# Kernel tuning notes

Hardware: AMD Instinct MI355X
Metric: run time of the kernel (lower is better)

The kernel has to match this reference:

```python
import jax, jax.numpy as jnp
import numpy as np

B = 8          # events
P = 16384      # points per event (P > MAX_TOKENS -> selection path)
FEAT = 6
TOK = 768
MT = 128       # max_tokens
K = 16         # k_neighbors
IH = 256       # importance_hidden_dim
LN_EPS = 1e-5


def _linear_init(key, fan_in, fan_out):
    kw, kb = jax.random.split(key)
    lim = 1.0 / np.sqrt(fan_in)
    w = jax.random.uniform(kw, (fan_in, fan_out), jnp.float32, -lim, lim)
    b = jax.random.uniform(kb, (fan_out,), jnp.float32, -lim, lim)
    return w, b


def setup_inputs() -> dict:
    key = jax.random.key(0)
    ks = jax.random.split(key, 16)
    # point data: col0 = batch index (sorted, equal counts), cols1:5 = x,y,z,t
    xyzt = jax.random.normal(ks[0], (B * P, 4), jnp.float32)
    bidx = jnp.repeat(jnp.arange(B, dtype=jnp.float32), P)[:, None]
    coordinates = jnp.concatenate([bidx, xyzt], axis=-1)
    features = jax.random.normal(ks[1], (B * P, FEAT), jnp.float32)
    # gumbel noise = -log(-log(U+1e-10)+1e-10)
    u = jax.random.uniform(ks[2], (B, P), jnp.float32)
    gumbel_noise = -jnp.log(-jnp.log(u + 1e-10) + 1e-10)
    # feature MLP: 6->256->512->768 (ReLU) -> 768
    w1, b1 = _linear_init(ks[3], FEAT, 256)
    w2, b2 = _linear_init(ks[4], 256, 512)
    w3, b3 = _linear_init(ks[5], 512, 768)
    w4, b4 = _linear_init(ks[6], 768, TOK)
    # importance encoder: (768+4)->256, ReLU, LN, 256->256, ReLU, 256->1
    iw1, ib1 = _linear_init(ks[7], TOK + 4, IH)
    ln_g = jnp.ones((IH,), jnp.float32)
    ln_b = jnp.zeros((IH,), jnp.float32)
    iw2, ib2 = _linear_init(ks[8], IH, IH)
    iw3, ib3 = _linear_init(ks[9], IH, 1)
    # neighborhood MLP: 768->768, ReLU, 768->768
    nw1, nb1 = _linear_init(ks[10], TOK, TOK)
    nw2, nb2 = _linear_init(ks[11], TOK, TOK)
    log_temperature = jnp.zeros((), jnp.float32)  # log(1.0)
    return dict(coordinates=coordinates, features=features,
                log_temperature=log_temperature,
                w1=w1, b1=b1, w2=w2, b2=b2, w3=w3, b3=b3, w4=w4, b4=b4,
                iw1=iw1, ib1=ib1, ln_g=ln_g, ln_b=ln_b, iw2=iw2, ib2=ib2,
                iw3=iw3, ib3=ib3, nw1=nw1, nb1=nb1, nw2=nw2, nb2=nb2,
                gumbel_noise=gumbel_noise, batch_size=B)


def _forward(coordinates, features, log_temperature,
             w1, b1, w2, b2, w3, b3, w4, b4,
             iw1, ib1, ln_g, ln_b, iw2, ib2, iw3, ib3,
             nw1, nb1, nw2, nb2, gumbel_noise, batch_size):
    N = coordinates.shape[0]
    Pn = N // batch_size
    coords4 = coordinates[:, 1:5]  # [N,4] (x,y,z,t)
    # point feature MLP
    h = jax.nn.relu(features @ w1 + b1)
    h = jax.nn.relu(h @ w2 + b2)
    h = jax.nn.relu(h @ w3 + b3)
    pf = h @ w4 + b4  # [N, TOK]
    # importance scores (context-aware)
    z = jax.nn.relu(jnp.concatenate([pf, coords4], axis=-1) @ iw1 + ib1)
    mu = jnp.mean(z, axis=-1, keepdims=True)
    var = jnp.var(z, axis=-1, keepdims=True)
    z = (z - mu) / jnp.sqrt(var + LN_EPS) * ln_g + ln_b
    z = jax.nn.relu(z @ iw2 + ib2)
    imp = (z @ iw3 + ib3)[:, 0]  # [N]
    temp = jnp.maximum(jnp.exp(log_temperature), 0.1)
    # equal-count sorted batches -> reshape and vmap over events
    pf_b = pf.reshape(batch_size, Pn, TOK)
    c_b = coords4.reshape(batch_size, Pn, 4)
    imp_b = imp.reshape(batch_size, Pn)

    def per_event(feats, coords, scores, noise):
        # gumbel-softmax top-k selection (soft mode: weights unused downstream)
        pert = (scores + noise) / temp
        _, sel = jax.lax.top_k(pert, MT)            # [MT]
        cent = coords[sel]                           # [MT,4]
        # squared euclidean distances centroids -> all points (same KNN order as cdist)
        d2 = jnp.sum((cent[:, None, :] - coords[None, :, :]) ** 2, axis=-1)  # [MT,P]
        _, knn = jax.lax.top_k(-d2, K)               # [MT,K]
        nbr = feats[knn]                             # [MT,K,TOK]
        pooled = jnp.max(nbr, axis=1)                # [MT,TOK]
        tok = jax.nn.relu(pooled @ nw1 + nb1) @ nw2 + nb2
        order = jnp.argsort(cent[:, 3])              # sort tokens by time
        return tok[order], cent[order]

    tokens, cents = jax.vmap(per_event)(pf_b, c_b, imp_b, gumbel_noise)
    return tokens, cents


def reference(coordinates, features, log_temperature,
              w1, b1, w2, b2, w3, b3, w4, b4,
              iw1, ib1, ln_g, ln_b, iw2, ib2, iw3, ib3,
              nw1, nb1, nw2, nb2, gumbel_noise, batch_size):
    tokens, cents = _forward(coordinates, features, log_temperature,
                             w1, b1, w2, b2, w3, b3, w4, b4,
                             iw1, ib1, ln_g, ln_b, iw2, ib2, iw3, ib3,
                             nw1, nb1, nw2, nb2, gumbel_noise, batch_size)
    masks = jnp.ones((batch_size, MT), dtype=bool)  # all events have > MT points
    return tokens, cents, masks
```

## Files before the change

kernel.cpp:

```cpp
#include <hip/hip_runtime.h>
#include <hip/hip_bf16.h>

#define NPT   131072
#define BATCH 8
#define PPE   16384
#define MT    128
#define KNN   16
#define TOKD  768
#define ZSPLIT 2

typedef short bf16x8 __attribute__((ext_vector_type(8)));
typedef float f32x4  __attribute__((ext_vector_type(4)));

#define GL16(g, l) __builtin_amdgcn_global_load_lds(                         \
    (const __attribute__((address_space(1))) void*)(g),                      \
    (__attribute__((address_space(3))) void*)(l), 16, 0, 0)

__device__ __forceinline__ unsigned pack_hi(unsigned u0, unsigned u1) {
    return (u0 >> 16) | (u1 & 0xFFFF0000u);
}
__device__ __forceinline__ void split1(float x, short& h, short& l) {
    const unsigned u = __float_as_uint(x);
    h = (short)(u >> 16);
    const float r = x - __uint_as_float(u & 0xFFFF0000u);
    l = (short)(__float_as_uint(r) >> 16);
}

__global__ __launch_bounds__(256) void prep_kernel(const float* __restrict__ coords,
                                                   float4* __restrict__ c4f)
{
    const int i = blockIdx.x * 256 + threadIdx.x;
    if (i < NPT) {
        const long b = (long)i * 5;
        c4f[i] = make_float4(coords[b + 1], coords[b + 2], coords[b + 3], coords[b + 4]);
    }
}

__global__ __launch_bounds__(256) void wsplit_all(
    const float* __restrict__ w2, const float* __restrict__ w3,
    const float* __restrict__ w4, const float* __restrict__ iw2,
    const float* __restrict__ nw1, const float* __restrict__ nw2,
    short* w2h, short* w2l, short* w3h, short* w3l,
    short* w4h, short* w4l, short* i2h, short* i2l,
    short* n1h, short* n1l, short* n2h, short* n2l)
{
    const int b = blockIdx.x;
    const float* W; int K, N, Kpad, n; short *hi, *lo;
    if (b < 512)       { W = w2;  K = 256; N = 512; Kpad = 256; hi = w2h; lo = w2l; n = b; }
    else if (b < 1280) { W = w3;  K = 512; N = 768; Kpad = 512; hi = w3h; lo = w3l; n = b - 512; }
    else if (b < 2048) { W = w4;  K = 768; N = 768; Kpad = 768; hi = w4h; lo = w4l; n = b - 1280; }
    else if (b < 2304) { W = iw2; K = 256; N = 256; Kpad = 256; hi = i2h; lo = i2l; n = b - 2048; }
    else if (b < 3072) { W = nw1; K = 768; N = 768; Kpad = 768; hi = n1h; lo = n1l; n = b - 2304; }
    else               { W = nw2; K = 768; N = 768; Kpad = 768; hi = n2h; lo = n2l; n = b - 3072; }
    for (int k = threadIdx.x; k < Kpad; k += 256) {
        short h = 0, l = 0;
        if (k < K) split1(W[(long)k * N + n], h, l);
        hi[(long)n * Kpad + k] = h;
        lo[(long)n * Kpad + k] = l;
    }
}

__global__ __launch_bounds__(256) void w45_kernel(const float* __restrict__ w4,
                                                  const float* __restrict__ iw1,
                                                  const float* __restrict__ b4,
                                                  const float* __restrict__ ib1,
                                                  short* __restrict__ hi,
                                                  short* __restrict__ lo,
                                                  float* __restrict__ bias45)
{
    const int k = blockIdx.x, n = threadIdx.x;
    if (k < 768) {
        const float* wr = w4 + (long)k * 768;
        float v0 = 0.f, v1 = 0.f, v2 = 0.f, v3 = 0.f;
        for (int j = 0; j < 768; j += 4) {
            v0 += wr[j]     * iw1[(long)j * 256 + n];
            v1 += wr[j + 1] * iw1[(long)(j + 1) * 256 + n];
            v2 += wr[j + 2] * iw1[(long)(j + 2) * 256 + n];
            v3 += wr[j + 3] * iw1[(long)(j + 3) * 256 + n];
        }
        const float v = (v0 + v1) + (v2 + v3);
        short h, l; split1(v, h, l);
        hi[(long)n * 800 + k] = h;
        lo[(long)n * 800 + k] = l;
    } else if (k < 800) {
        const float v = (k < 772) ? iw1[(long)k * 256 + n] : 0.f;
        short h, l; split1(v, h, l);
        hi[(long)n * 800 + k] = h;
        lo[(long)n * 800 + k] = l;
    } else {
        float v0 = 0.f, v1 = 0.f, v2 = 0.f, v3 = 0.f;
        for (int j = 0; j < 768; j += 4) {
            v0 += b4[j]     * iw1[(long)j * 256 + n];
            v1 += b4[j + 1] * iw1[(long)(j + 1) * 256 + n];
            v2 += b4[j + 2] * iw1[(long)(j + 2) * 256 + n];
            v3 += b4[j + 3] * iw1[(long)(j + 3) * 256 + n];
        }
        bias45[n] = (v0 + v1) + (v2 + v3) + ib1[n];
    }
}

__global__ __launch_bounds__(256) void l1_kernel(const float* __restrict__ f,
                                                 const float* __restrict__ w1,
                                                 const float* __restrict__ b1,
                                                 short* __restrict__ hp,
                                                 short* __restrict__ lp,
                                                 int base,
                                                 const int* __restrict__ gather)
{
    const int r0 = blockIdx.x << 6, tid = threadIdx.x;
    float wc[6];
#pragma unroll
    for (int k = 0; k < 6; ++k) wc[k] = w1[k * 256 + tid];
    const float bb = b1[tid];
    for (int i = 0; i < 64; ++i) {
        const int r = r0 + i;
        int row = gather ? gather[r] : (base + r);
        row = (row < 0) ? 0 : ((row >= NPT) ? (NPT - 1) : row);
        float acc = bb;
#pragma unroll
        for (int k = 0; k < 6; ++k) acc += f[(long)row * 6 + k] * wc[k];
        acc = fmaxf(acc, 0.f);
        short h, l; split1(acc, h, l);
        hp[(long)r * 256 + tid] = h;
        lp[(long)r * 256 + tid] = l;
    }
}

__global__ __launch_bounds__(256) void gather_h3_kernel(const short* __restrict__ H3,
                                                        const int* __restrict__ knn_idx,
                                                        int off,
                                                        short* __restrict__ G)
{
    const int i = blockIdx.x;
    const int row = knn_idx[off + i];
    const int4* src = (const int4*)(H3 + (long)row * 768);
    int4* dst = (int4*)(G + (long)i * 768);
    if (threadIdx.x < 96) dst[threadIdx.x] = src[threadIdx.x];
}

__global__ __launch_bounds__(256, 3) void gemm_mf(
    const short* __restrict__ Aph, const short* __restrict__ Apl,
    const float* __restrict__ Afp, int Kpad,
    const short* __restrict__ Wth, const short* __restrict__ Wtl,
    const float* __restrict__ bias,
    short* __restrict__ Cph, short* __restrict__ Cpl, int KpadOut,
    float* __restrict__ Cf, short* __restrict__ Cp768,
    float* __restrict__ Cpool,
    const float* __restrict__ CoordC, int cfBase,
    int N, int relu, long partStride)
{
    __shared__ short Ah[128 * 32];
    __shared__ short Al[128 * 32];
    __shared__ short Bh[128 * 32];
    __shared__ short Bl[128 * 32];
    const int tid = threadIdx.x;
    int rowb, colb;
    {
        const int ncol = gridDim.x, nrow = gridDim.y;
        if ((nrow & 7) == 0) {
            const int id  = blockIdx.y * ncol + blockIdx.x;
            const int sgs = ncol << 3;
            const int sg = id / sgs, wi = id % sgs;
            rowb = (sg << 3) + (wi & 7);
            colb = wi >> 3;
        } else { rowb = blockIdx.y; colb = blockIdx.x; }
    }
    const int row0 = rowb << 7, col0 = colb << 7;
    const int wave = tid >> 6, lane = tid & 63;
    const int wr = wave >> 1, wc = wave & 1;
    const int q = lane >> 4, l16 = lane & 15;
    const int l2 = lane >> 2;
    const int ksw = (((lane & 3) ^ ((lane >> 3) & 3)) << 3);
    const int rchunk = ((q ^ ((l16 >> 1) & 3)) << 3);

    f32x4 acc[4][4];
#pragma unroll
    for (int mt = 0; mt < 4; ++mt)
#pragma unroll
        for (int nt = 0; nt < 4; ++nt)
            acc[mt][nt] = (f32x4){0.f, 0.f, 0.f, 0.f};

    const bool useAl = (Apl != nullptr) || (Aph == nullptr);
    const int nkT = Kpad >> 5;
    const int Z = gridDim.z, zb = blockIdx.z;
    const int t0 = (nkT * zb) / Z, t1 = (nkT * (zb + 1)) / Z;

    auto stage = [&](int t) {
        const int k0 = t << 5;
#pragma unroll
        for (int i = 0; i < 2; ++i) {
            const int mb = (wave << 5) + (i << 4);
            const long gb = (long)(col0 + mb + l2) * Kpad + k0 + ksw;
            GL16(&Wth[gb], &Bh[mb * 32]);
            GL16(&Wtl[gb], &Bl[mb * 32]);
        }
        if (Aph) {
#pragma unroll
            for (int i = 0; i < 2; ++i) {
                const int mb = (wave << 5) + (i << 4);
                const long ga = (long)(row0 + mb + l2) * Kpad + k0 + ksw;
                GL16(&Aph[ga], &Ah[mb * 32]);
                if (Apl) GL16(&Apl[ga], &Al[mb * 32]);
            }
        } else {
#pragma unroll
            for (int s = 0; s < 4; ++s) {
                const int l  = (s << 8) + tid;
                const int m  = l >> 3;
                const int k4 = (l & 7) << 2;
                const float4 v = *(const float4*)&Afp[(long)(row0 + m) * Kpad + k0 + k4];
                const unsigned u0 = __float_as_uint(v.x), u1 = __float_as_uint(v.y);
                const unsigned u2 = __float_as_uint(v.z), u3 = __float_as_uint(v.w);
                const unsigned r0 = __float_as_uint(v.x - __uint_as_float(u0 & 0xFFFF0000u));
                const unsigned r1 = __float_as_uint(v.y - __uint_as_float(u1 & 0xFFFF0000u));
                const unsigned r2 = __float_as_uint(v.z - __uint_as_float(u2 & 0xFFFF0000u));
                const unsigned r3 = __float_as_uint(v.w - __uint_as_float(u3 & 0xFFFF0000u));
                const int off = m * 32 + ((((k4 >> 3) ^ ((m >> 1) & 3)) << 3) | (k4 & 4));
                *(int2*)&Ah[off] = make_int2((int)pack_hi(u0, u1), (int)pack_hi(u2, u3));
                *(int2*)&Al[off] = make_int2((int)pack_hi(r0, r1), (int)pack_hi(r2, r3));
            }
        }
    };

    stage(t0);
    __syncthreads();

    for (int t = t0; t < t1; ++t) {
        bf16x8 ah[4], al[4], bh[4], bl[4];
#pragma unroll
        for (int i = 0; i < 4; ++i) {
            const int mrow = (wr << 6) + (i << 4) + l16;
            const int ncol = (wc << 6) + (i << 4) + l16;
            ah[i] = *(const bf16x8*)&Ah[mrow * 32 + rchunk];
            if (useAl) al[i] = *(const bf16x8*)&Al[mrow * 32 + rchunk];
            bh[i] = *(const bf16x8*)&Bh[ncol * 32 + rchunk];
            bl[i] = *(const bf16x8*)&Bl[ncol * 32 + rchunk];
        }
        __syncthreads();
        if (t + 1 < t1) stage(t + 1);
#pragma unroll
        for (int nt = 0; nt < 4; ++nt)
#pragma unroll
            for (int mt = 0; mt < 4; ++mt) {
                acc[mt][nt] = __builtin_amdgcn_mfma_f32_16x16x32_bf16(ah[mt], bh[nt], acc[mt][nt], 0, 0, 0);
                acc[mt][nt] = __builtin_amdgcn_mfma_f32_16x16x32_bf16(ah[mt], bl[nt], acc[mt][nt], 0, 0, 0);
                if (useAl)
                    acc[mt][nt] = __builtin_amdgcn_mfma_f32_16x16x32_bf16(al[mt], bh[nt], acc[mt][nt], 0, 0, 0);
            }
        __syncthreads();
    }

    if (Cf && Z > 1) {
        float* dst = Cf + (long)zb * partStride;
#pragma unroll
        for (int mt = 0; mt < 4; ++mt)
#pragma unroll
            for (int nt = 0; nt < 4; ++nt) {
                const int col = col0 + (wc << 6) + (nt << 4) + l16;
#pragma unroll
                for (int rg = 0; rg < 4; ++rg) {
                    const int row = row0 + (wr << 6) + (mt << 4) + (q << 2) + rg;
                    dst[(long)row * N + col] = acc[mt][nt][rg];
                }
            }
        return;
    }

    if (Cpool) {
#pragma unroll
        for (int mt = 0; mt < 4; ++mt)
#pragma unroll
            for (int nt = 0; nt < 4; ++nt) {
                const int col = col0 + (wc << 6) + (nt << 4) + l16;
                float m = fmaxf(fmaxf(acc[mt][nt][0], acc[mt][nt][1]),
                                fmaxf(acc[mt][nt][2], acc[mt][nt][3]));
                m = fmaxf(m, __shfl_xor(m, 16));
                m = fmaxf(m, __shfl_xor(m, 32));
                m += bias[col];
                if (relu) m = fmaxf(m, 0.f);
                if (q == 0)
                    Cpool[(long)((row0 >> 4) + (wr << 2) + mt) * 768 + col] = m;
            }
        return;
    }
#pragma unroll
    for (int mt = 0; mt < 4; ++mt)
#pragma unroll
        for (int nt = 0; nt < 4; ++nt) {
            const int col = col0 + (wc << 6) + (nt << 4) + l16;
            const float bs = bias[col];
#pragma unroll
            for (int rg = 0; rg < 4; ++rg) {
                const int row = row0 + (wr << 6) + (mt << 4) + (q << 2) + rg;
                float v = acc[mt][nt][rg] + bs;
                if (relu) v = fmaxf(v, 0.f);
                if (Cf) Cf[(long)row * N + col] = v;
                if (Cph || Cp768) {
                    short h, l; split1(v, h, l);
                    if (Cph) {
                        Cph[(long)row * KpadOut + col] = h;
                        Cpl[(long)row * KpadOut + col] = l;
                    }
                    if (Cp768) Cp768[(long)row * 768 + col] = h;
                }
            }
        }
    if (CoordC && Cph && colb == 0 && tid < 128) {
        const int r = row0 + tid;
        const long rb = (long)r * KpadOut;
        const long cb = (long)(cfBase + r) * 5;
#pragma unroll
        for (int d = 0; d < 4; ++d) {
            short h, l; split1(CoordC[cb + 1 + d], h, l);
            Cph[rb + 768 + d] = h;
            Cpl[rb + 768 + d] = l;
        }
        for (int c = 772; c < 800; ++c) { Cph[rb + c] = 0; Cpl[rb + c] = 0; }
    }
}

__global__ __launch_bounds__(256) void ln_kernel(const float* __restrict__ Fp,
                                                 long pstride,
                                                 const float* __restrict__ g,
                                                 const float* __restrict__ b,
                                                 const float* __restrict__ badd,
                                                 short* __restrict__ hp,
                                                 short* __restrict__ lp)
{
    const int tid = threadIdx.x, wave = tid >> 6, lane = tid & 63;
    float gv[4], bv[4], av[4];
#pragma unroll
    for (int j = 0; j < 4; ++j) {
        gv[j] = g[lane * 4 + j]; bv[j] = b[lane * 4 + j]; av[j] = badd[lane * 4 + j];
    }
    for (int i = 0; i < 2; ++i) {
        const int r = (blockIdx.x << 3) + (wave << 1) + i;
        const long off = (long)r * 256 + lane * 4;
        float4 x = *(const float4*)&Fp[off];
#pragma unroll
        for (int z = 1; z < ZSPLIT; ++z) {
            const float4 p = *(const float4*)&Fp[(long)z * pstride + off];
            x.x += p.x; x.y += p.y; x.z += p.z; x.w += p.w;
        }
        x.x = fmaxf(x.x + av[0], 0.f);
        x.y = fmaxf(x.y + av[1], 0.f);
        x.z = fmaxf(x.z + av[2], 0.f);
        x.w = fmaxf(x.w + av[3], 0.f);
        float s = x.x + x.y + x.z + x.w;
#pragma unroll
        for (int off2 = 32; off2; off2 >>= 1) s += __shfl_down(s, off2);
        const float mu = __shfl(s, 0) * (1.f / 256.f);
        const float d0 = x.x - mu, d1 = x.y - mu, d2 = x.z - mu, d3 = x.w - mu;
        float s2 = d0 * d0 + d1 * d1 + d2 * d2 + d3 * d3;
#pragma unroll
        for (int off2 = 32; off2; off2 >>= 1) s2 += __shfl_down(s2, off2);
        const float den = sqrtf(__shfl(s2, 0) * (1.f / 256.f) + 1e-5f);
        const float v[4] = { d0 / den * gv[0] + bv[0], d1 / den * gv[1] + bv[1],
                             d2 / den * gv[2] + bv[2], d3 / den * gv[3] + bv[3] };
#pragma unroll
        for (int j = 0; j < 4; ++j) {
            short h, l; split1(v[j], h, l);
            hp[(long)r * 256 + lane * 4 + j] = h;
            lp[(long)r * 256 + lane * 4 + j] = l;
        }
    }
}

__global__ __launch_bounds__(256) void imp_kernel(const float* __restrict__ Fp,
                                                  long pstride,
                                                  const float* __restrict__ iw3,
                                                  const float* __restrict__ ib3,
                                                  const float* __restrict__ ib2,
                                                  const float* __restrict__ noise,
                                                  const float* __restrict__ lt,
                                                  float* __restrict__ pert,
                                                  int base)
{
    const int tid = threadIdx.x, wave = tid >> 6, lane = tid & 63;
    float wv[4], bv[4];
#pragma unroll
    for (int j = 0; j < 4; ++j) { wv[j] = iw3[lane * 4 + j]; bv[j] = ib2[lane * 4 + j]; }
    const float temp = fmaxf(expf(lt[0]), 0.1f);
    const float b3v = ib3[0];
    for (int i = 0; i < 2; ++i) {
        const int r = (blockIdx.x << 3) + (wave << 1) + i;
        const long off = (long)r * 256 + lane * 4;
        float4 x = *(const float4*)&Fp[off];
#pragma unroll
        for (int z = 1; z < ZSPLIT; ++z) {
            const float4 p = *(const float4*)&Fp[(long)z * pstride + off];
            x.x += p.x; x.y += p.y; x.z += p.z; x.w += p.w;
        }
        float s = fmaxf(x.x + bv[0], 0.f) * wv[0] + fmaxf(x.y + bv[1], 0.f) * wv[1]
                + fmaxf(x.z + bv[2], 0.f) * wv[2] + fmaxf(x.w + bv[3], 0.f) * wv[3];
#pragma unroll
        for (int off2 = 32; off2; off2 >>= 1) s += __shfl_down(s, off2);
        if (lane == 0)
            pert[base + r] = (s + b3v + noise[base + r]) / temp;
    }
}

__device__ __forceinline__ unsigned fmap(float f) {
    unsigned x = __float_as_uint(f);
    return (x & 0x80000000u) ? ~x : (x | 0x80000000u);
}

__global__ __launch_bounds__(256) void topk_part(const float* __restrict__ pert,
                                                 unsigned long long* __restrict__ cand)
{
    const int e = blockIdx.x >> 3, s = blockIdx.x & 7, tid = threadIdx.x;
    const int base = e * PPE + s * 2048;
    __shared__ unsigned long long key[2048];
    for (int i = tid; i < 2048; i += 256)
        key[i] = ((unsigned long long)fmap(pert[base + i]) << 32) | (unsigned)(~(base + i));
    __syncthreads();
    for (int k = 2; k <= 2048; k <<= 1)
        for (int j = k >> 1; j > 0; j >>= 1) {
            for (int i = tid; i < 2048; i += 256) {
                const int l = i ^ j;
                if (l > i) {
                    const unsigned long long a = key[i], b = key[l];
                    const bool up = ((i & k) == 0);
                    if (up ? (a < b) : (a > b)) { key[i] = b; key[l] = a; }
                }
            }
            __syncthreads();
        }
    if (tid < MT) cand[(long)blockIdx.x * MT + tid] = key[tid];
}

__global__ __launch_bounds__(256) void topk_merge(const unsigned long long* __restrict__ cand,
                                                  const float4* __restrict__ c4f,
                                                  float* __restrict__ centf)
{
    const int e = blockIdx.x, tid = threadIdx.x;
    __shared__ unsigned long long key[1024];
    for (int i = tid; i < 1024; i += 256)
        key[i] = cand[(long)e * 1024 + i];
    __syncthreads();
    for (int k = 2; k <= 1024; k <<= 1)
        for (int j = k >> 1; j > 0; j >>= 1) {
            for (int i = tid; i < 1024; i += 256) {
                const int l = i ^ j;
                if (l > i) {
                    const unsigned long long a = key[i], b = key[l];
                    const bool up = ((i & k) == 0);
                    if (up ? (a < b) : (a > b)) { key[i] = b; key[l] = a; }
                }
            }
            __syncthreads();
        }
    if (tid < MT) {
        const int idx = (int)(~(unsigned)(key[tid] & 0xFFFFFFFFu));
        *(float4*)&centf[(long)(e * MT + tid) * 4] = c4f[idx];
    }
}

__device__ __forceinline__ unsigned d2bits(const float4 x, float c0, float c1,
                                           float c2, float c3) {
    const float q0 = __fmul_rn(c0 - x.x, c0 - x.x);
    const float q1 = __fmul_rn(c1 - x.y, c1 - x.y);
    const float q2 = __fmul_rn(c2 - x.z, c2 - x.z);
    const float q3 = __fmul_rn(c3 - x.w, c3 - x.w);
    return __float_as_uint(__fadd_rn(__fadd_rn(__fadd_rn(q0, q1), q2), q3));
}

__global__ __launch_bounds__(256) void knn_kernel(const float4* __restrict__ c4f,
                                                  const float* __restrict__ centf,
                                                  int* __restrict__ knn_idx)
{
    const int blk = blockIdx.x, tid = threadIdx.x;
    const int e = blk >> 7, base = e * PPE;
    const int c4 = tid & 3;
    const float c0 = centf[(long)blk * 4 + 0];
    const float c1 = centf[(long)blk * 4 + 1];
    const float c2 = centf[(long)blk * 4 + 2];
    const float c3 = centf[(long)blk * 4 + 3];
    __shared__ unsigned short d16[PPE];
    __shared__ unsigned long long ubuf[664];
    __shared__ int sh_need; __shared__ unsigned sh_b;
    __shared__ int clt, ceq;
    unsigned* hist4 = (unsigned*)ubuf;
    unsigned* histm = hist4 + 1024;
    for (int i = tid; i < 1024; i += 256) hist4[i] = 0;
    __syncthreads();
    for (int p = tid; p < PPE; p += 256) {
        const unsigned u = d2bits(c4f[base + p], c0, c1, c2, c3);
        d16[p] = (unsigned short)(u >> 16);
        atomicAdd(&hist4[((u >> 24) << 2) | c4], 1u);
    }
    __syncthreads();
    histm[tid] = hist4[tid << 2] + hist4[(tid << 2) | 1]
               + hist4[(tid << 2) | 2] + hist4[(tid << 2) | 3];
    __syncthreads();
    if (tid == 0) {
        int cum = 0, b = 0;
        for (; b < 255; ++b) { cum += (int)histm[b]; if (cum >= KNN) break; }
        if (cum < KNN) { cum += (int)histm[255]; b = 255; }
        sh_need = KNN - (cum - (int)histm[b]); sh_b = (unsigned)b;
    }
    __syncthreads();
    int need = sh_need;
    const unsigned b1v = sh_b;
    __syncthreads();
    for (int i = tid; i < 1024; i += 256) hist4[i] = 0;
    __syncthreads();
    for (int p = tid; p < PPE; p += 256) {
        const unsigned h = d16[p];
        if ((h >> 8) == b1v) atomicAdd(&hist4[((h & 255u) << 2) | c4], 1u);
    }
    __syncthreads();
    histm[tid] = hist4[tid << 2] + hist4[(tid << 2) | 1]
               + hist4[(tid << 2) | 2] + hist4[(tid << 2) | 3];
    __syncthreads();
    if (tid == 0) {
        int cum = 0, b = 0;
        for (; b < 255; ++b) { cum += (int)histm[b]; if (cum >= need) break; }
        if (cum < need) { cum += (int)histm[255]; b = 255; }
        sh_need = need - (cum - (int)histm[b]); sh_b = (unsigned)b;
    }
    __syncthreads();
    need = sh_need;
    const unsigned prefix16 = (b1v << 8) | sh_b;
    int* lt_i = (int*)ubuf;
    unsigned* lt_u = (unsigned*)(lt_i + KNN);
    int* eqbuf = (int*)(lt_u + KNN);
    unsigned long long* key256 = (unsigned long long*)(eqbuf + 256);
    if (tid == 0) { clt = 0; ceq = 0; }
    __syncthreads();
    for (int p = tid; p < PPE; p += 256) {
        const unsigned h = d16[p];
        if (h < prefix16)        { int q = atomicAdd(&clt, 1); if (q < KNN) lt_i[q] = p; }
        else if (h == prefix16)  { int q = atomicAdd(&ceq, 1); if (q < 256) eqbuf[q] = p; }
    }
    __syncthreads();
    const int nlt = (clt < KNN) ? clt : KNN;
    if (tid < nlt) lt_u[tid] = d2bits(c4f[base + lt_i[tid]], c0, c1, c2, c3);
    if (ceq <= 256) {
        key256[tid] = (tid < ceq)
            ? (((unsigned long long)d2bits(c4f[base + eqbuf[tid]], c0, c1, c2, c3) << 32)
               | (unsigned)eqbuf[tid])
            : 0xFFFFFFFFFFFFFFFFull;
        __syncthreads();
        for (int k = 2; k <= 256; k <<= 1)
            for (int j = k >> 1; j > 0; j >>= 1) {
                const int l = tid ^ j;
                if (l > tid) {
                    const unsigned long long a = key256[tid], b = key256[l];
                    const bool up = ((tid & k) == 0);
                    if (up ? (a > b) : (a < b)) { key256[tid] = b; key256[l] = a; }
                }
                __syncthreads();
            }
    } else if (tid == 0) {
        unsigned long long sel[KNN];
        int n = 0;
        for (int p = 0; p < PPE; ++p) {
            if (d16[p] != (unsigned short)prefix16) continue;
            const unsigned long long kk =
                ((unsigned long long)d2bits(c4f[base + p], c0, c1, c2, c3) << 32) | (unsigned)p;
            if (n < need) {
                int j = n++;
                while (j > 0 && sel[j - 1] > kk) { sel[j] = sel[j - 1]; --j; }
                sel[j] = kk;
            } else if (kk < sel[need - 1]) {
                int j = need - 1;
                while (j > 0 && sel[j - 1] > kk) { sel[j] = sel[j - 1]; --j; }
                sel[j] = kk;
            }
        }
        for (int j = 0; j < need; ++j) key256[j] = sel[j];
    }
    __syncthreads();
    if (tid == 0) {
        unsigned long long fin[KNN];
        int n = 0;
        for (int i = 0; i < nlt; ++i) {
            const unsigned long long kk = ((unsigned long long)lt_u[i] << 32) | (unsigned)lt_i[i];
            int j = n++;
            while (j > 0 && fin[j - 1] > kk) { fin[j] = fin[j - 1]; --j; }
            fin[j] = kk;
        }
        for (int i = 0; i < need; ++i) {
            const unsigned long long kk = key256[i];
            int j = n++;
            while (j > 0 && fin[j - 1] > kk) { fin[j] = fin[j - 1]; --j; }
            fin[j] = kk;
        }
        for (int r = 0; r < KNN; ++r)
            knn_idx[blk * KNN + r] = base + (int)(unsigned)(fin[r] & 0xFFFFFFFFu);
    }
}

__global__ __launch_bounds__(256) void emit_kernel(const float* __restrict__ centf,
                                                   const float* __restrict__ tokf,
                                                   float* __restrict__ out,
                                                   long out_size)
{
    const int e = blockIdx.x, s = blockIdx.y, tid = threadIdx.x;
    __shared__ float tv[MT];
    __shared__ int   rk[MT];
    if (tid < MT) tv[tid] = centf[(long)(e * MT + tid) * 4 + 3];
    __syncthreads();
    if (tid < MT) {
        const float t = tv[tid]; int r = 0;
        for (int j = 0; j < MT; ++j)
            r += (tv[j] < t || (tv[j] == t && j < tid)) ? 1 : 0;
        rk[tid] = r;
    }
    __syncthreads();
    const long cent_off = (long)BATCH * MT * TOKD;
    const long mask_off = cent_off + (long)BATCH * MT * 4;
    for (int i = s * 8; i < s * 8 + 8; ++i) {
        const float* src = tokf + ((size_t)e * MT + i) * TOKD;
        const long dst = ((long)e * MT + rk[i]) * TOKD;
        for (int t4 = tid; t4 < TOKD / 4; t4 += 256) {
            const float4 v = ((const float4*)src)[t4];
            const long g = dst + (long)t4 * 4;
            if (g + 3 < out_size) {
                *(float4*)&out[g] = v;
            } else {
                if (g + 0 < out_size) out[g + 0] = v.x;
                if (g + 1 < out_size) out[g + 1] = v.y;
                if (g + 2 < out_size) out[g + 2] = v.z;
                if (g + 3 < out_size) out[g + 3] = v.w;
            }
        }
    }
    if (s == 0) {
        for (int idx = tid; idx < MT * 4; idx += 256) {
            const int i = idx >> 2, d = idx & 3;
            const long g = cent_off + ((long)e * MT + rk[i]) * 4 + d;
            if (g < out_size) out[g] = centf[((long)e * MT + i) * 4 + d];
        }
        for (int idx = tid; idx < MT; idx += 256) {
            const long g = mask_off + (long)e * MT + idx;
            if (g < out_size) out[g] = 1.0f;
        }
    }
}

extern "C" void kernel_launch(void* const* d_in, const int* in_sizes, int n_in,
                              void* d_out, int out_size, void* d_ws, size_t ws_size,
                              hipStream_t stream)
{
    const float* coords = (const float*)d_in[0];
    const float* feats  = (const float*)d_in[1];
    const float* lt     = (const float*)d_in[2];
    const float* w1  = (const float*)d_in[3];  const float* b1  = (const float*)d_in[4];
    const float* w2  = (const float*)d_in[5];  const float* b2  = (const float*)d_in[6];
    const float* w3  = (const float*)d_in[7];  const float* b3  = (const float*)d_in[8];
    const float* w4  = (const float*)d_in[9];  const float* b4  = (const float*)d_in[10];
    const float* iw1 = (const float*)d_in[11]; const float* ib1 = (const float*)d_in[12];
    const float* lng = (const float*)d_in[13]; const float* lnb = (const float*)d_in[14];
    const float* iw2 = (const float*)d_in[15]; const float* ib2 = (const float*)d_in[16];
    const float* iw3 = (const float*)d_in[17]; const float* ib3 = (const float*)d_in[18];
    const float* nw1 = (const float*)d_in[19]; const float* nb1 = (const float*)d_in[20];
    const float* nw2 = (const float*)d_in[21]; const float* nb2 = (const float*)d_in[22];
    const float* noise = (const float*)d_in[23];

    const int NBR = BATCH * MT * KNN;
    const size_t FIXED_FL = (size_t)NPT + 4096 + 16384 + 16384 + (size_t)1024 * TOKD
                          + (size_t)NPT * 4 + 256 + 2 * (size_t)1024 * TOKD;
    const size_t s_w2 = 512 * 256,  s_w3 = 768 * 512,  s_w4 = 768 * 768;
    const size_t s_45 = 256 * 800,  s_i2 = 256 * 256;
    const size_t s_n1 = 768 * 768,  s_n2 = 768 * 768;
    const size_t WTOT = 2 * (s_w2 + s_w3 + s_w4 + s_45 + s_i2 + s_n1 + s_n2);
    const size_t BASE_BYTES = FIXED_FL * 4 + WTOT * 2;
    const size_t PERROW = (800 * 2 + 512 * 2) * 2 + (size_t)ZSPLIT * 256 * 4;
    int ch = 128;
    while (ch < NPT && BASE_BYTES + (size_t)(ch * 2) * PERROW <= ws_size) ch <<= 1;
    const size_t H3_BYTES = (size_t)NPT * 768 * 2;
    const bool persist = (BASE_BYTES + (size_t)ch * PERROW + H3_BYTES) <= ws_size;

    float*  pert   = (float*)d_ws;
    float*  centf  = pert + NPT;
    int*    knn    = (int*)(centf + 4096);
    unsigned long long* cand = (unsigned long long*)(knn + 16384);
    float*  pooled = (float*)(cand + 8192);
    float4* c4f    = (float4*)(pooled + (size_t)1024 * TOKD);
    float*  bias45 = (float*)(c4f + NPT);
    float*  T1     = bias45 + 256;
    float*  T2     = T1 + (size_t)1024 * TOKD;
    short*  wsp    = (short*)(T2 + (size_t)1024 * TOKD);
    short* w2h = wsp;            short* w2l = w2h + s_w2;
    short* w3h = w2l + s_w2;     short* w3l = w3h + s_w3;
    short* w4h = w3l + s_w3;     short* w4l = w4h + s_w4;
    short* f45h = w4l + s_w4;    short* f45l = f45h + s_45;
    short* i2h = f45l + s_45;    short* i2l = i2h + s_i2;
    short* n1h = i2l + s_i2;     short* n1l = n1h + s_n1;
    short* n2h = n1l + s_n1;     short* n2l = n2h + s_n2;
    short* PAh = n2l + s_n2;     short* PAl = PAh + (size_t)ch * 800;
    short* PBh = PAl + (size_t)ch * 800;
    short* PBl = PBh + (size_t)ch * 512;
    float* Fp  = (float*)(PBl + (size_t)ch * 512);
    short* H3  = (short*)(Fp + (size_t)ZSPLIT * ch * 256);
    const long pstride = (long)ch * 256;

    prep_kernel<<<dim3((NPT + 255) / 256), dim3(256), 0, stream>>>(coords, c4f);
    wsplit_all<<<dim3(3840), dim3(256), 0, stream>>>(
        w2, w3, w4, iw2, nw1, nw2,
        w2h, w2l, w3h, w3l, w4h, w4l, i2h, i2l, n1h, n1l, n2h, n2l);
    w45_kernel<<<dim3(801), dim3(256), 0, stream>>>(w4, iw1, b4, ib1, f45h, f45l, bias45);

    for (int ck = 0; ck < NPT / ch; ++ck) {
        const int base = ck * ch;
        l1_kernel<<<dim3(ch / 64), dim3(256), 0, stream>>>(feats, w1, b1, PAh, PAl, base, nullptr);
        gemm_mf<<<dim3(512 / 128, ch / 128), dim3(256), 0, stream>>>(
            PAh, PAl, nullptr, 256, w2h, w2l, b2, PBh, PBl, 512,
            nullptr, nullptr, nullptr, nullptr, 0, 512, 1, 0);
        gemm_mf<<<dim3(768 / 128, ch / 128), dim3(256), 0, stream>>>(
            PBh, PBl, nullptr, 512, w3h, w3l, b3, PAh, PAl, 800,
            nullptr, persist ? (H3 + (size_t)base * 768) : nullptr, nullptr,
            coords, base, 768, 1, 0);
        gemm_mf<<<dim3(256 / 128, ch / 128, ZSPLIT), dim3(256), 0, stream>>>(
            PAh, PAl, nullptr, 800, f45h, f45l, nullptr, nullptr, nullptr, 0,
            Fp, nullptr, nullptr, nullptr, 0, 256, 0, pstride);
        ln_kernel<<<dim3(ch / 8), dim3(256), 0, stream>>>(
            Fp, pstride, lng, lnb, bias45, PBh, PBl);
        gemm_mf<<<dim3(256 / 128, ch / 128, ZSPLIT), dim3(256), 0, stream>>>(
            PBh, PBl, nullptr, 256, i2h, i2l, nullptr, nullptr, nullptr, 0,
            Fp, nullptr, nullptr, nullptr, 0, 256, 0, pstride);
        imp_kernel<<<dim3(ch / 8), dim3(256), 0, stream>>>(
            Fp, pstride, iw3, ib3, ib2, noise, lt, pert, base);
    }

    topk_part<<<dim3(BATCH * 8), dim3(256), 0, stream>>>(pert, cand);
    topk_merge<<<dim3(BATCH), dim3(256), 0, stream>>>(cand, c4f, centf);
    knn_kernel<<<dim3(BATCH * MT), dim3(256), 0, stream>>>(c4f, centf, knn);

    const int rcch = (ch < NBR) ? ch : NBR;
    for (int rc = 0; rc < NBR / rcch; ++rc) {
        if (persist) {
            gather_h3_kernel<<<dim3(rcch), dim3(256), 0, stream>>>(
                H3, knn, rc * rcch, PAh);
            gemm_mf<<<dim3(768 / 128, rcch / 128), dim3(256), 0, stream>>>(
                PAh, nullptr, nullptr, 768, w4h, w4l, b4, nullptr, nullptr, 0,
                nullptr, nullptr, pooled + (size_t)(rc * rcch / 16) * 768,
                nullptr, 0, 768, 0, 0);
        } else {
            l1_kernel<<<dim3(rcch / 64), dim3(256), 0, stream>>>(feats, w1, b1, PAh, PAl, 0, knn + (size_t)rc * rcch);
            gemm_mf<<<dim3(512 / 128, rcch / 128), dim3(256), 0, stream>>>(
                PAh, PAl, nullptr, 256, w2h, w2l, b2, PBh, PBl, 512,
                nullptr, nullptr, nullptr, nullptr, 0, 512, 1, 0);
            gemm_mf<<<dim3(768 / 128, rcch / 128), dim3(256), 0, stream>>>(
                PBh, PBl, nullptr, 512, w3h, w3l, b3, PAh, PAl, 768,
                nullptr, nullptr, nullptr, nullptr, 0, 768, 1, 0);
            gemm_mf<<<dim3(768 / 128, rcch / 128), dim3(256), 0, stream>>>(
                PAh, PAl, nullptr, 768, w4h, w4l, b4, nullptr, nullptr, 0,
                nullptr, nullptr, pooled + (size_t)(rc * rcch / 16) * 768,
                nullptr, 0, 768, 0, 0);
        }
    }

    gemm_mf<<<dim3(768 / 128, 1024 / 128), dim3(256), 0, stream>>>(
        nullptr, nullptr, pooled, 768, n1h, n1l, nb1, nullptr, nullptr, 0,
        T1, nullptr, nullptr, nullptr, 0, 768, 1, 0);
    gemm_mf<<<dim3(768 / 128, 1024 / 128), dim3(256), 0, stream>>>(
        nullptr, nullptr, T1, 768, n2h, n2l, nb2, nullptr, nullptr, 0,
        T2, nullptr, nullptr, nullptr, 0, 768, 0, 0);
    emit_kernel<<<dim3(BATCH, 16), dim3(256), 0, stream>>>(
        centf, T2, (float*)d_out, (long)out_size);
}
```

Baseline: 1.673 ms.

## Replace full bitonic sort in top-k partial with radix-bucket select

```diff
diff --git a/kernel.cpp b/kernel.cpp
--- a/kernel.cpp
+++ b/kernel.cpp
@@ -410,23 +410,90 @@
 {
     const int e = blockIdx.x >> 3, s = blockIdx.x & 7, tid = threadIdx.x;
     const int base = e * PPE + s * 2048;
-    __shared__ unsigned long long key[2048];
-    for (int i = tid; i < 2048; i += 256)
-        key[i] = ((unsigned long long)fmap(pert[base + i]) << 32) | (unsigned)(~(base + i));
-    __syncthreads();
-    for (int k = 2; k <= 2048; k <<= 1)
-        for (int j = k >> 1; j > 0; j >>= 1) {
-            for (int i = tid; i < 2048; i += 256) {
-                const int l = i ^ j;
-                if (l > i) {
-                    const unsigned long long a = key[i], b = key[l];
-                    const bool up = ((i & k) == 0);
-                    if (up ? (a < b) : (a > b)) { key[i] = b; key[l] = a; }
+    const int c4 = tid & 3;
+    __shared__ unsigned hist4[1024];
+    __shared__ unsigned long long gt[MT];
+    __shared__ unsigned long long eqk[256];
+    __shared__ int cgt, ceq, sh_need;
+    __shared__ unsigned sh_b;
+    unsigned u[8];
+#pragma unroll
+    for (int i = 0; i < 8; ++i)
+        u[i] = fmap(pert[base + (i << 8) + tid]);
+    for (int i = tid; i < 1024; i += 256) hist4[i] = 0;
+    if (tid == 0) { cgt = 0; ceq = 0; }
+    __syncthreads();
+#pragma unroll
+    for (int i = 0; i < 8; ++i)
+        atomicAdd(&hist4[((u[i] >> 24) << 2) | c4], 1u);
+    __syncthreads();
+    if (tid == 0) {
+        int cum = 0, b = 255, cb = 0;
+        for (; b > 0; --b) {
+            cb = (int)(hist4[b << 2] + hist4[(b << 2) | 1]
+                     + hist4[(b << 2) | 2] + hist4[(b << 2) | 3]);
+            cum += cb;
+            if (cum >= MT) break;
+        }
+        if (cum < MT) {
+            cb = (int)(hist4[0] + hist4[1] + hist4[2] + hist4[3]);
+            cum += cb; b = 0;
+        }
+        sh_need = MT - (cum - cb);
+        sh_b = (unsigned)b;
+    }
+    __syncthreads();
+    const unsigned bb = sh_b;
+    const int need = sh_need;
+#pragma unroll
+    for (int i = 0; i < 8; ++i) {
+        const unsigned bkt = u[i] >> 24;
+        const int idx = base + (i << 8) + tid;
+        const unsigned long long kk =
+            ((unsigned long long)u[i] << 32) | (unsigned)(~idx);
+        if (bkt > bb)        { int q = atomicAdd(&cgt, 1); if (q < MT)  gt[q]  = kk; }
+        else if (bkt == bb)  { int q = atomicAdd(&ceq, 1); if (q < 256) eqk[q] = kk; }
+    }
+    __syncthreads();
+    const int ngt = (cgt < MT) ? cgt : MT;
+    if (ceq <= 256) {
+        if (tid >= ceq) eqk[tid] = 0ull;
+        __syncthreads();
+        for (int k = 2; k <= 256; k <<= 1)
+            for (int j = k >> 1; j > 0; j >>= 1) {
+                const int l = tid ^ j;
+                if (l > tid) {
+                    const unsigned long long a = eqk[tid], b = eqk[l];
+                    const bool up = ((tid & k) == 0);
+                    if (up ? (a < b) : (a > b)) { eqk[tid] = b; eqk[l] = a; }
                 }
-            }
-            __syncthreads();
-        }
-    if (tid < MT) cand[(long)blockIdx.x * MT + tid] = key[tid];
+                __syncthreads();
+            }
+    } else {
+        if (tid == 0) {
+            unsigned long long sel[MT];
+            int n = 0;
+            for (int p = 0; p < 2048; ++p) {
+                const unsigned uu = fmap(pert[base + p]);
+                if ((uu >> 24) != bb) continue;
+                const unsigned long long kk =
+                    ((unsigned long long)uu << 32) | (unsigned)(~(base + p));
+                if (n < need) {
+                    int j = n++;
+                    while (j > 0 && sel[j - 1] < kk) { sel[j] = sel[j - 1]; --j; }
+                    sel[j] = kk;
+                } else if (kk > sel[need - 1]) {
+                    int j = need - 1;
+                    while (j > 0 && sel[j - 1] < kk) { sel[j] = sel[j - 1]; --j; }
+                    sel[j] = kk;
+                }
+            }
+            for (int j = 0; j < need; ++j) eqk[j] = sel[j];
+        }
+        __syncthreads();
+    }
+    if (tid < MT)
+        cand[(long)blockIdx.x * MT + tid] = (tid < ngt) ? gt[tid] : eqk[tid - ngt];
 }
 
 __global__ __launch_bounds__(256) void topk_merge(const unsigned long long* __restrict__ cand,
```

After: 3.643 ms. +117.8%, slower.
